# Kernel optimization log

Measured on AMD Instinct MI355X. Metric: run time of the kernel, lower is better.

Reference implementation:

```python
import jax, jax.numpy as jnp
import numpy as np

N_NODES = 16384   # n_features in the torch code (graph nodes)
N_EDGES = 262144  # nnz of sparse Laplacian (avg degree 16)
K = 4             # receptive_field_k (Chebyshev order)
F_OUT = 32        # gconv_filter_size
BATCH = 256       # n_batch


def setup_inputs() -> dict:
    key = jax.random.key(0)
    k1, k2, k3, k4, k5, k6 = jax.random.split(key, 6)
    x = jax.random.normal(k1, (BATCH, N_NODES), dtype=jnp.float32)
    rows = jax.random.randint(k2, (N_EDGES,), 0, N_NODES)
    cols = jax.random.randint(k3, (N_EDGES,), 0, N_NODES)
    vals = jax.random.normal(k4, (N_EDGES,), dtype=jnp.float32) * 0.1
    bound = 1.0 / np.sqrt(K)  # kaiming-uniform-ish init bound, fan_in = K
    weight = jax.random.uniform(k5, (F_OUT, K), minval=-bound, maxval=bound, dtype=jnp.float32)
    bias = jax.random.uniform(k6, (F_OUT,), minval=-bound, maxval=bound, dtype=jnp.float32)
    return dict(x=x, vals=vals, rows=rows, cols=cols, weight=weight, bias=bias)


def _spmm(vals, rows, cols, xT):
    # sparse L @ xT with xT: (N, B); edge-wise gather then segment-sum scatter
    contrib = vals[:, None] * xT[cols]  # (E, B)
    return jax.ops.segment_sum(contrib, rows, num_segments=N_NODES)


def reference(x, vals, rows, cols, weight, bias):
    # Scaled Laplacian: Lhat = 2*L/lmax - I; normalized Laplacian has lmax=2 -> Lhat = L - I
    xT = x.T  # (N, B)

    def lhat(v):
        return _spmm(vals, rows, cols, v) - v

    # Chebyshev recurrence: T0 = x, T1 = Lhat x, Tk = 2 Lhat T_{k-1} - T_{k-2}
    t0 = xT
    t1 = lhat(t0)
    terms = [t0, t1]
    for _ in range(K - 2):
        terms.append(2.0 * lhat(terms[-1]) - terms[-2])
    xk = jnp.stack(terms, axis=0)  # (K, N, B)

    # original stacks (K, B, N), permutes (1,2,0) -> (B, N, K), reshape -> (B*N, K)
    feats = jnp.transpose(xk, (2, 1, 0)).reshape(BATCH * N_NODES, K)
    y = feats @ weight.T + bias  # F.linear
    return y.reshape(BATCH, N_NODES, F_OUT)
```

## Files before the change

### kernel.cpp

```cpp
#include <hip/hip_runtime.h>

#define N_NODES 16384
#define N_EDGES 262144
#define BATCH   256
#define F_OUT   32
#define K_ORD   4
#define NCHUNK  4
#define CHUNK   64
#define NPB     8

typedef float f32x4 __attribute__((ext_vector_type(4)));
typedef float f32x2 __attribute__((ext_vector_type(2)));

__device__ __forceinline__ unsigned short f2bf(float f) {
    unsigned u = __float_as_uint(f);
    return (unsigned short)((u + 0x7FFFu + ((u >> 16) & 1u)) >> 16);
}
__device__ __forceinline__ float bf2f(unsigned v) {
    return __uint_as_float(v << 16);
}

__global__ void transpose_kernel(const float* __restrict__ x, float* __restrict__ xT,
                                 unsigned short* __restrict__ xb) {
    __shared__ float tile[32][33];
    int tx = threadIdx.x;
    int ty = threadIdx.y;
    int n0 = blockIdx.x * 32;
    int b0 = blockIdx.y * 32;
#pragma unroll
    for (int j = 0; j < 4; ++j) {
        int b = b0 + ty + j * 8;
        int n = n0 + tx;
        tile[ty + j * 8][tx] = x[(size_t)b * N_NODES + n];
    }
    __syncthreads();
#pragma unroll
    for (int j = 0; j < 4; ++j) {
        int n = n0 + ty + j * 8;
        int b = b0 + tx;
        float v = tile[tx][ty + j * 8];
        xT[(size_t)n * BATCH + b] = v;
        xb[(size_t)n * BATCH + b] = f2bf(v);
    }
}

__global__ void hist_kernel(const int* __restrict__ rows, int* __restrict__ count) {
    int e = blockIdx.x * blockDim.x + threadIdx.x;
    if (e < N_EDGES) atomicAdd(&count[rows[e]], 1);
}

__global__ void scan_kernel(int* __restrict__ count, int* __restrict__ row_ptr) {
    __shared__ int part[256];
    int t = threadIdx.x;
    int base = t * 64;
    int loc[64];
    int s = 0;
#pragma unroll
    for (int i = 0; i < 64; ++i) { loc[i] = count[base + i]; s += loc[i]; }
    part[t] = s;
    __syncthreads();
    for (int d = 1; d < 256; d <<= 1) {
        int v = (t >= d) ? part[t - d] : 0;
        __syncthreads();
        part[t] += v;
        __syncthreads();
    }
    int off = part[t] - s;
#pragma unroll
    for (int i = 0; i < 64; ++i) {
        row_ptr[base + i] = off;
        count[base + i] = off;
        off += loc[i];
    }
    if (t == 255) row_ptr[N_NODES] = off;
}

__global__ void scatter_kernel(const int* __restrict__ rows, const int* __restrict__ cols,
                               const float* __restrict__ vals,
                               int* __restrict__ cursor,
                               unsigned* __restrict__ csrp) {
    int e = blockIdx.x * blockDim.x + threadIdx.x;
    if (e < N_EDGES) {
        int r = rows[e];
        int pos = atomicAdd(&cursor[r], 1);
        csrp[pos] = (unsigned)cols[e] | ((unsigned)f2bf(vals[e]) << 16);
    }
}

__global__ void cheb_kernel(const float* __restrict__ in, const unsigned short* __restrict__ inb,
                            const float* __restrict__ prev,
                            float* __restrict__ out, unsigned short* __restrict__ outb,
                            const int* __restrict__ row_ptr,
                            const unsigned* __restrict__ csrp, float c) {
    int chunk = blockIdx.x & (NCHUNK - 1);
    int ng    = blockIdx.x >> 2;
    int nsub  = threadIdx.x >> 5;
    int b     = chunk * CHUNK + (threadIdx.x & 31) * 2;
    int n     = ng * NPB + nsub;
    int beg = row_ptr[n], end = row_ptr[n + 1];
    f32x2 acc = (f32x2)(0.f);
    int e = beg;
    for (; e + 3 < end; e += 4) {
        unsigned p0 = csrp[e], p1 = csrp[e + 1], p2 = csrp[e + 2], p3 = csrp[e + 3];
        unsigned g0 = *(const unsigned*)&inb[(size_t)(p0 & 0xFFFF) * BATCH + b];
        unsigned g1 = *(const unsigned*)&inb[(size_t)(p1 & 0xFFFF) * BATCH + b];
        unsigned g2 = *(const unsigned*)&inb[(size_t)(p2 & 0xFFFF) * BATCH + b];
        unsigned g3 = *(const unsigned*)&inb[(size_t)(p3 & 0xFFFF) * BATCH + b];
        float v0 = bf2f(p0 >> 16), v1 = bf2f(p1 >> 16), v2 = bf2f(p2 >> 16), v3 = bf2f(p3 >> 16);
        acc.x += v0 * bf2f(g0 & 0xFFFF) + v1 * bf2f(g1 & 0xFFFF)
               + v2 * bf2f(g2 & 0xFFFF) + v3 * bf2f(g3 & 0xFFFF);
        acc.y += v0 * bf2f(g0 >> 16) + v1 * bf2f(g1 >> 16)
               + v2 * bf2f(g2 >> 16) + v3 * bf2f(g3 >> 16);
    }
    for (; e < end; ++e) {
        unsigned p = csrp[e];
        unsigned g = *(const unsigned*)&inb[(size_t)(p & 0xFFFF) * BATCH + b];
        float v = bf2f(p >> 16);
        acc.x += v * bf2f(g & 0xFFFF);
        acc.y += v * bf2f(g >> 16);
    }
    size_t idx = (size_t)n * BATCH + b;
    f32x2 self = *(const f32x2*)&in[idx];
    f32x2 o = c * (acc - self);
    if (prev) o -= *(const f32x2*)&prev[idx];
    *(f32x2*)&out[idx] = o;
    *(unsigned*)&outb[idx] = (unsigned)f2bf(o.x) | ((unsigned)f2bf(o.y) << 16);
}

__global__ void final_kernel(const float* __restrict__ t0, const float* __restrict__ t1,
                             const float* __restrict__ t2, const unsigned short* __restrict__ t2b,
                             const int* __restrict__ row_ptr,
                             const unsigned* __restrict__ csrp,
                             const float* __restrict__ weight, const float* __restrict__ bias,
                             float* __restrict__ out) {
    __shared__ float w[F_OUT * K_ORD];
    __shared__ float bb[F_OUT];
    __shared__ f32x4 tval[NPB][CHUNK + 1];
    int tid = threadIdx.x;
    if (tid < F_OUT * K_ORD) w[tid] = weight[tid];
    if (tid < F_OUT) bb[tid] = bias[tid];
    __syncthreads();

    int chunk = blockIdx.x & (NCHUNK - 1);
    int ng    = blockIdx.x >> 2;
    {
        int nsub = tid >> 5;
        int bi   = (tid & 31) * 2;
        int b    = chunk * CHUNK + bi;
        int n    = ng * NPB + nsub;
        int beg = row_ptr[n], end = row_ptr[n + 1];
        f32x2 acc = (f32x2)(0.f);
        int e = beg;
        for (; e + 3 < end; e += 4) {
            unsigned p0 = csrp[e], p1 = csrp[e + 1], p2 = csrp[e + 2], p3 = csrp[e + 3];
            unsigned g0 = *(const unsigned*)&t2b[(size_t)(p0 & 0xFFFF) * BATCH + b];
            unsigned g1 = *(const unsigned*)&t2b[(size_t)(p1 & 0xFFFF) * BATCH + b];
            unsigned g2 = *(const unsigned*)&t2b[(size_t)(p2 & 0xFFFF) * BATCH + b];
            unsigned g3 = *(const unsigned*)&t2b[(size_t)(p3 & 0xFFFF) * BATCH + b];
            float v0 = bf2f(p0 >> 16), v1 = bf2f(p1 >> 16), v2 = bf2f(p2 >> 16), v3 = bf2f(p3 >> 16);
            acc.x += v0 * bf2f(g0 & 0xFFFF) + v1 * bf2f(g1 & 0xFFFF)
                   + v2 * bf2f(g2 & 0xFFFF) + v3 * bf2f(g3 & 0xFFFF);
            acc.y += v0 * bf2f(g0 >> 16) + v1 * bf2f(g1 >> 16)
                   + v2 * bf2f(g2 >> 16) + v3 * bf2f(g3 >> 16);
        }
        for (; e < end; ++e) {
            unsigned p = csrp[e];
            unsigned g = *(const unsigned*)&t2b[(size_t)(p & 0xFFFF) * BATCH + b];
            float v = bf2f(p >> 16);
            acc.x += v * bf2f(g & 0xFFFF);
            acc.y += v * bf2f(g >> 16);
        }
        size_t idx = (size_t)n * BATCH + b;
        f32x2 t2v = *(const f32x2*)&t2[idx];
        f32x2 t1v = *(const f32x2*)&t1[idx];
        f32x2 t0v = *(const f32x2*)&t0[idx];
        f32x2 t3v = 2.f * (acc - t2v) - t1v;
        tval[nsub][bi]     = (f32x4){t0v.x, t1v.x, t2v.x, t3v.x};
        tval[nsub][bi + 1] = (f32x4){t0v.y, t1v.y, t2v.y, t3v.y};
    }
    __syncthreads();

    int f = (tid & 7) * 4;
    f32x4 w0 = *(const f32x4*)&w[(f + 0) * 4];
    f32x4 w1 = *(const f32x4*)&w[(f + 1) * 4];
    f32x4 w2 = *(const f32x4*)&w[(f + 2) * 4];
    f32x4 w3 = *(const f32x4*)&w[(f + 3) * 4];
    f32x4 b4 = *(const f32x4*)&bb[f];
    int nsub = (tid >> 3) & 7;
    int wv   = tid >> 6;
    size_t n = (size_t)(ng * NPB + nsub);
#pragma unroll
    for (int i = 0; i < 16; ++i) {
        int b_idx = i * 4 + wv;
        size_t b  = (size_t)(chunk * CHUNK + b_idx);
        f32x4 tv = tval[nsub][b_idx];
        f32x4 r;
        r.x = w0.x * tv.x + w0.y * tv.y + w0.z * tv.z + w0.w * tv.w + b4.x;
        r.y = w1.x * tv.x + w1.y * tv.y + w1.z * tv.z + w1.w * tv.w + b4.y;
        r.z = w2.x * tv.x + w2.y * tv.y + w2.z * tv.z + w2.w * tv.w + b4.z;
        r.w = w3.x * tv.x + w3.y * tv.y + w3.z * tv.z + w3.w * tv.w + b4.w;
        __builtin_nontemporal_store(r, (f32x4*)(out + (b * N_NODES + n) * F_OUT + f));
    }
}

extern "C" void kernel_launch(void* const* d_in, const int* in_sizes, int n_in,
                              void* d_out, int out_size, void* d_ws, size_t ws_size,
                              hipStream_t stream) {
    const float* x      = (const float*)d_in[0];
    const float* vals   = (const float*)d_in[1];
    const int*   rows   = (const int*)d_in[2];
    const int*   cols   = (const int*)d_in[3];
    const float* weight = (const float*)d_in[4];
    const float* bias   = (const float*)d_in[5];
    float* out = (float*)d_out;

    const size_t NB = (size_t)N_NODES * BATCH;
    float*          xT      = (float*)d_ws;
    float*          t1      = xT + NB;
    float*          t2      = t1 + NB;
    unsigned short* xb      = (unsigned short*)(t2 + NB);
    unsigned short* t1b     = xb + NB;
    unsigned short* t2b     = t1b + NB;
    int*            row_ptr = (int*)(t2b + NB);
    int*            cursor  = row_ptr + 16448;
    unsigned*       csrp    = (unsigned*)(cursor + N_NODES);

    (void)hipMemsetAsync(cursor, 0, N_NODES * sizeof(int), stream);

    transpose_kernel<<<dim3(N_NODES / 32, BATCH / 32), dim3(32, 8), 0, stream>>>(x, xT, xb);
    hist_kernel<<<N_EDGES / 256, 256, 0, stream>>>(rows, cursor);
    scan_kernel<<<1, 256, 0, stream>>>(cursor, row_ptr);
    scatter_kernel<<<N_EDGES / 256, 256, 0, stream>>>(rows, cols, vals, cursor, csrp);

    const int GRID = (N_NODES / NPB) * NCHUNK;
    cheb_kernel<<<GRID, 256, 0, stream>>>(xT, xb, nullptr, t1, t1b, row_ptr, csrp, 1.f);
    cheb_kernel<<<GRID, 256, 0, stream>>>(t1, t1b, xT, t2, t2b, row_ptr, csrp, 2.f);
    final_kernel<<<GRID, 256, 0, stream>>>(xT, t1, t2, t2b, row_ptr, csrp,
                                           weight, bias, out);
}
```

Before: 214.4 us.

## Make final kernel persistent with double-buffered tiles and read bf16 copies of T0/T1

The final kernel now runs on a fixed grid of 2048 blocks, and each block loops over several node groups. A double-buffered shared tile lets the SpMM gather for the next group run after the current group's output stores are issued. T0 and T1 are read from their bf16 copies instead of fp32, both in the final kernel and as the prev term in the second Chebyshev step, which cuts read bandwidth but adds rounding error to the output. Launch bounds are also added to the final kernel.

```diff
diff --git a/kernel.cpp b/kernel.cpp
--- a/kernel.cpp
+++ b/kernel.cpp
@@ -8,6 +8,10 @@
 #define NCHUNK  4
 #define CHUNK   64
 #define NPB     8
+#define GRID_F  2048
+#define NGRP    (N_NODES / NPB)
+#define SLOTS   (GRID_F / NCHUNK)
+#define GPB_F   (NGRP / SLOTS)
 
 typedef float f32x4 __attribute__((ext_vector_type(4)));
 typedef float f32x2 __attribute__((ext_vector_type(2)));
@@ -88,7 +92,7 @@
 }
 
 __global__ void cheb_kernel(const float* __restrict__ in, const unsigned short* __restrict__ inb,
-                            const float* __restrict__ prev,
+                            const unsigned short* __restrict__ prevb,
                             float* __restrict__ out, unsigned short* __restrict__ outb,
                             const int* __restrict__ row_ptr,
                             const unsigned* __restrict__ csrp, float c) {
@@ -122,41 +126,56 @@
     size_t idx = (size_t)n * BATCH + b;
     f32x2 self = *(const f32x2*)&in[idx];
     f32x2 o = c * (acc - self);
-    if (prev) o -= *(const f32x2*)&prev[idx];
+    if (prevb) {
+        unsigned pv = *(const unsigned*)&prevb[idx];
+        o.x -= bf2f(pv & 0xFFFF);
+        o.y -= bf2f(pv >> 16);
+    }
     *(f32x2*)&out[idx] = o;
     *(unsigned*)&outb[idx] = (unsigned)f2bf(o.x) | ((unsigned)f2bf(o.y) << 16);
 }
 
-__global__ void final_kernel(const float* __restrict__ t0, const float* __restrict__ t1,
-                             const float* __restrict__ t2, const unsigned short* __restrict__ t2b,
-                             const int* __restrict__ row_ptr,
-                             const unsigned* __restrict__ csrp,
-                             const float* __restrict__ weight, const float* __restrict__ bias,
-                             float* __restrict__ out) {
+__global__ void __launch_bounds__(256, 8)
+final_kernel(const unsigned short* __restrict__ t0b, const unsigned short* __restrict__ t1b,
+             const float* __restrict__ t2, const unsigned short* __restrict__ t2b,
+             const int* __restrict__ row_ptr,
+             const unsigned* __restrict__ csrp,
+             const float* __restrict__ weight, const float* __restrict__ bias,
+             float* __restrict__ out) {
     __shared__ float w[F_OUT * K_ORD];
     __shared__ float bb[F_OUT];
-    __shared__ f32x4 tval[NPB][CHUNK + 1];
+    __shared__ f32x4 tval[2][NPB][CHUNK + 1];
     int tid = threadIdx.x;
     if (tid < F_OUT * K_ORD) w[tid] = weight[tid];
     if (tid < F_OUT) bb[tid] = bias[tid];
     __syncthreads();
 
     int chunk = blockIdx.x & (NCHUNK - 1);
-    int ng    = blockIdx.x >> 2;
-    {
-        int nsub = tid >> 5;
-        int bi   = (tid & 31) * 2;
-        int b    = chunk * CHUNK + bi;
-        int n    = ng * NPB + nsub;
+    int bslot = blockIdx.x >> 2;
+
+    int p1_nsub = tid >> 5;
+    int p1_bi   = (tid & 31) * 2;
+    int p1_b    = chunk * CHUNK + p1_bi;
+    int f = (tid & 7) * 4;
+    f32x4 w0 = *(const f32x4*)&w[(f + 0) * 4];
+    f32x4 w1 = *(const f32x4*)&w[(f + 1) * 4];
+    f32x4 w2 = *(const f32x4*)&w[(f + 2) * 4];
+    f32x4 w3 = *(const f32x4*)&w[(f + 3) * 4];
+    f32x4 b4 = *(const f32x4*)&bb[f];
+    int p2_nsub = (tid >> 3) & 7;
+    int p2_wv   = tid >> 6;
+
+    auto phase1 = [&](int g, int buf) {
+        int n = (bslot + g * SLOTS) * NPB + p1_nsub;
         int beg = row_ptr[n], end = row_ptr[n + 1];
         f32x2 acc = (f32x2)(0.f);
         int e = beg;
         for (; e + 3 < end; e += 4) {
             unsigned p0 = csrp[e], p1 = csrp[e + 1], p2 = csrp[e + 2], p3 = csrp[e + 3];
-            unsigned g0 = *(const unsigned*)&t2b[(size_t)(p0 & 0xFFFF) * BATCH + b];
-            unsigned g1 = *(const unsigned*)&t2b[(size_t)(p1 & 0xFFFF) * BATCH + b];
-            unsigned g2 = *(const unsigned*)&t2b[(size_t)(p2 & 0xFFFF) * BATCH + b];
-            unsigned g3 = *(const unsigned*)&t2b[(size_t)(p3 & 0xFFFF) * BATCH + b];
+            unsigned g0 = *(const unsigned*)&t2b[(size_t)(p0 & 0xFFFF) * BATCH + p1_b];
+            unsigned g1 = *(const unsigned*)&t2b[(size_t)(p1 & 0xFFFF) * BATCH + p1_b];
+            unsigned g2 = *(const unsigned*)&t2b[(size_t)(p2 & 0xFFFF) * BATCH + p1_b];
+            unsigned g3 = *(const unsigned*)&t2b[(size_t)(p3 & 0xFFFF) * BATCH + p1_b];
             float v0 = bf2f(p0 >> 16), v1 = bf2f(p1 >> 16), v2 = bf2f(p2 >> 16), v3 = bf2f(p3 >> 16);
             acc.x += v0 * bf2f(g0 & 0xFFFF) + v1 * bf2f(g1 & 0xFFFF)
                    + v2 * bf2f(g2 & 0xFFFF) + v3 * bf2f(g3 & 0xFFFF);
@@ -165,41 +184,40 @@
         }
         for (; e < end; ++e) {
             unsigned p = csrp[e];
-            unsigned g = *(const unsigned*)&t2b[(size_t)(p & 0xFFFF) * BATCH + b];
+            unsigned g = *(const unsigned*)&t2b[(size_t)(p & 0xFFFF) * BATCH + p1_b];
             float v = bf2f(p >> 16);
             acc.x += v * bf2f(g & 0xFFFF);
             acc.y += v * bf2f(g >> 16);
         }
-        size_t idx = (size_t)n * BATCH + b;
+        size_t idx = (size_t)n * BATCH + p1_b;
         f32x2 t2v = *(const f32x2*)&t2[idx];
-        f32x2 t1v = *(const f32x2*)&t1[idx];
-        f32x2 t0v = *(const f32x2*)&t0[idx];
+        unsigned u0 = *(const unsigned*)&t0b[idx];
+        unsigned u1 = *(const unsigned*)&t1b[idx];
+        f32x2 t0v = {bf2f(u0 & 0xFFFF), bf2f(u0 >> 16)};
+        f32x2 t1v = {bf2f(u1 & 0xFFFF), bf2f(u1 >> 16)};
         f32x2 t3v = 2.f * (acc - t2v) - t1v;
-        tval[nsub][bi]     = (f32x4){t0v.x, t1v.x, t2v.x, t3v.x};
-        tval[nsub][bi + 1] = (f32x4){t0v.y, t1v.y, t2v.y, t3v.y};
-    }
-    __syncthreads();
-
-    int f = (tid & 7) * 4;
-    f32x4 w0 = *(const f32x4*)&w[(f + 0) * 4];
-    f32x4 w1 = *(const f32x4*)&w[(f + 1) * 4];
-    f32x4 w2 = *(const f32x4*)&w[(f + 2) * 4];
-    f32x4 w3 = *(const f32x4*)&w[(f + 3) * 4];
-    f32x4 b4 = *(const f32x4*)&bb[f];
-    int nsub = (tid >> 3) & 7;
-    int wv   = tid >> 6;
-    size_t n = (size_t)(ng * NPB + nsub);
-#pragma unroll
-    for (int i = 0; i < 16; ++i) {
-        int b_idx = i * 4 + wv;
-        size_t b  = (size_t)(chunk * CHUNK + b_idx);
-        f32x4 tv = tval[nsub][b_idx];
-        f32x4 r;
-        r.x = w0.x * tv.x + w0.y * tv.y + w0.z * tv.z + w0.w * tv.w + b4.x;
-        r.y = w1.x * tv.x + w1.y * tv.y + w1.z * tv.z + w1.w * tv.w + b4.y;
-        r.z = w2.x * tv.x + w2.y * tv.y + w2.z * tv.z + w2.w * tv.w + b4.z;
-        r.w = w3.x * tv.x + w3.y * tv.y + w3.z * tv.z + w3.w * tv.w + b4.w;
-        __builtin_nontemporal_store(r, (f32x4*)(out + (b * N_NODES + n) * F_OUT + f));
+        tval[buf][p1_nsub][p1_bi]     = (f32x4){t0v.x, t1v.x, t2v.x, t3v.x};
+        tval[buf][p1_nsub][p1_bi + 1] = (f32x4){t0v.y, t1v.y, t2v.y, t3v.y};
+    };
+
+    phase1(0, 0);
+    for (int g = 0; g < GPB_F; ++g) {
+        __syncthreads();
+        size_t n = (size_t)((bslot + g * SLOTS) * NPB + p2_nsub);
+        int buf = g & 1;
+#pragma unroll
+        for (int i = 0; i < 16; ++i) {
+            int b_idx = i * 4 + p2_wv;
+            size_t b  = (size_t)(chunk * CHUNK + b_idx);
+            f32x4 tv = tval[buf][p2_nsub][b_idx];
+            f32x4 r;
+            r.x = w0.x * tv.x + w0.y * tv.y + w0.z * tv.z + w0.w * tv.w + b4.x;
+            r.y = w1.x * tv.x + w1.y * tv.y + w1.z * tv.z + w1.w * tv.w + b4.y;
+            r.z = w2.x * tv.x + w2.y * tv.y + w2.z * tv.z + w2.w * tv.w + b4.z;
+            r.w = w3.x * tv.x + w3.y * tv.y + w3.z * tv.z + w3.w * tv.w + b4.w;
+            __builtin_nontemporal_store(r, (f32x4*)(out + (b * N_NODES + n) * F_OUT + f));
+        }
+        if (g + 1 < GPB_F) phase1(g + 1, (g + 1) & 1);
     }
 }
 
@@ -234,7 +252,7 @@
 
     const int GRID = (N_NODES / NPB) * NCHUNK;
     cheb_kernel<<<GRID, 256, 0, stream>>>(xT, xb, nullptr, t1, t1b, row_ptr, csrp, 1.f);
-    cheb_kernel<<<GRID, 256, 0, stream>>>(t1, t1b, xT, t2, t2b, row_ptr, csrp, 2.f);
-    final_kernel<<<GRID, 256, 0, stream>>>(xT, t1, t2, t2b, row_ptr, csrp,
-                                           weight, bias, out);
-}
+    cheb_kernel<<<GRID, 256, 0, stream>>>(t1, t1b, xb, t2, t2b, row_ptr, csrp, 2.f);
+    final_kernel<<<GRID_F, 256, 0, stream>>>(xb, t1b, t2, t2b, row_ptr, csrp,
+                                             weight, bias, out);
+}
```

Result: slower. 244.3 us (+14.0%).
